# Kernel optimization log

Measured on AMD Instinct MI355X. Metric: run time of the kernel, lower is better.

## Reference

```python
import jax, jax.numpy as jnp
import numpy as np

# 3x3 window hardcoded in the original forward (symmetric, so corr == conv)
_WINDOW = np.array([[0.09474166, 0.11831801, 0.09474166],
                    [0.11831801, 0.14776132, 0.11831801],
                    [0.09474166, 0.11831801, 0.09474166]], dtype=np.float32)


def _filt(img, kern):
    # img: [B,1,H,W], kern: [1,1,3,3]; SAME padding (cv2 border effects are
    # confined to a 1-px rim, which the [5:-5,5:-5] crop removes anyway)
    return jax.lax.conv_general_dilated(
        img, kern, window_strides=(1, 1), padding='SAME',
        dimension_numbers=('NCHW', 'OIHW', 'NCHW'))


def setup_inputs() -> dict:
    key = jax.random.key(0)
    k1, k2 = jax.random.split(key)
    B, C, H, W = 64, 1, 512, 512
    X = jax.random.uniform(k1, (B, C, H, W), dtype=jnp.float32)
    Y = jax.random.uniform(k2, (B, C, H, W), dtype=jnp.float32)
    return {"X": X, "Y": Y}


def reference(X, Y):
    kern = jnp.asarray(_WINDOW)[None, None]  # [1,1,3,3]
    crop = lambda t: t[:, 0, 5:-5, 5:-5]      # channel 0, crop 5-px border

    mu1 = crop(_filt(X, kern))
    mu2 = crop(_filt(Y, kern))
    sigma1_sq = crop(_filt(X * X, kern)) - mu1 * mu1
    sigma2_sq = crop(_filt(Y * Y, kern)) - mu2 * mu2
    sigma12 = crop(_filt(X * Y, kern)) - mu1 * mu2

    # per-sample loss = mean over cropped HW; batch_loss = sum over samples
    loss = sigma1_sq * sigma2_sq - 2.0 * sigma12  # [B, H-10, W-10]
    return jnp.sum(jnp.mean(loss, axis=(1, 2)))
```

## Files before the change

### kernel.cpp

```cpp
#include <hip/hip_runtime.h>

#define A_W 0.30780133f
#define B_W 0.38439735f

#define IMG_W 512
#define CROP_LO 5
#define CROP_HI 507
#define STRIP 32
#define NSTRIPS 16
#define NCOLBLK 2
#define BLOCK_THREADS 256

struct Raw6 { float xl, xc, xr, yl, yc, yr; };
struct H5   { float s1, s2, s11, s22, s12; };

__device__ __forceinline__ Raw6 ld_row(const float* __restrict__ Xb,
                                       const float* __restrict__ Yb,
                                       int row, int c) {
    const float* Xr = Xb + (size_t)row * IMG_W;
    const float* Yr = Yb + (size_t)row * IMG_W;
    Raw6 r;
    r.xl = Xr[c - 1]; r.xc = Xr[c]; r.xr = Xr[c + 1];
    r.yl = Yr[c - 1]; r.yc = Yr[c]; r.yr = Yr[c + 1];
    return r;
}

__device__ __forceinline__ H5 hsum(const Raw6& r) {
    H5 h;
    h.s1  = A_W * (r.xl + r.xr)               + B_W * r.xc;
    h.s2  = A_W * (r.yl + r.yr)               + B_W * r.yc;
    h.s11 = A_W * (r.xl * r.xl + r.xr * r.xr) + B_W * (r.xc * r.xc);
    h.s22 = A_W * (r.yl * r.yl + r.yr * r.yr) + B_W * (r.yc * r.yc);
    h.s12 = A_W * (r.xl * r.yl + r.xr * r.yr) + B_W * (r.xc * r.yc);
    return h;
}

__global__ __launch_bounds__(BLOCK_THREADS) void ssim_loss_main(
    const float* __restrict__ X, const float* __restrict__ Y,
    float* __restrict__ partials) {
    const int t  = threadIdx.x;
    const int c  = CROP_LO + blockIdx.x * BLOCK_THREADS + t;
    const int cc = min(c, IMG_W - 2);
    const float vm = (c < CROP_HI) ? 1.0f : 0.0f;
    const int b  = blockIdx.z;
    const int i0 = CROP_LO + blockIdx.y * STRIP;

    const float* Xb = X + (size_t)b * IMG_W * IMG_W;
    const float* Yb = Y + (size_t)b * IMG_W * IMG_W;

    Raw6 rA = ld_row(Xb, Yb, i0 - 1, cc);
    Raw6 rB = ld_row(Xb, Yb, i0,     cc);
    Raw6 rC = ld_row(Xb, Yb, i0 + 1, cc);
    Raw6 rD = ld_row(Xb, Yb, i0 + 2, cc);
    H5 P = hsum(rA);
    H5 C = hsum(rB);

    float acc = 0.0f;
#pragma unroll
    for (int r = 0; r < STRIP; ++r) {
        Raw6 rNew = ld_row(Xb, Yb, min(i0 + r + 3, IMG_W - 1), cc);

        H5 N = hsum(rC);

        float s1  = A_W * (P.s1  + N.s1)  + B_W * C.s1;
        float s2  = A_W * (P.s2  + N.s2)  + B_W * C.s2;
        float s11 = A_W * (P.s11 + N.s11) + B_W * C.s11;
        float s22 = A_W * (P.s22 + N.s22) + B_W * C.s22;
        float s12 = A_W * (P.s12 + N.s12) + B_W * C.s12;

        float v1 = s11 - s1 * s1;
        float v2 = s22 - s2 * s2;
        float cv = s12 - s1 * s2;
        float term = v1 * v2 - 2.0f * cv;

        acc += (i0 + r < CROP_HI) ? vm * term : 0.0f;

        P = C; C = N; rC = rD; rD = rNew;
    }

    for (int off = 32; off > 0; off >>= 1) acc += __shfl_down(acc, off, 64);
    __shared__ float wsum[BLOCK_THREADS / 64];
    if ((t & 63) == 0) wsum[t >> 6] = acc;
    __syncthreads();
    if (t == 0)
        partials[blockIdx.x + NCOLBLK * (blockIdx.y + NSTRIPS * blockIdx.z)] =
            wsum[0] + wsum[1] + wsum[2] + wsum[3];
}

__global__ __launch_bounds__(256) void ssim_loss_finalize(
    const float* __restrict__ partials, int n, float* __restrict__ out) {
    const int tid = threadIdx.x;
    float s = 0.0f;
    for (int i = tid; i < n; i += 256) s += partials[i];
    for (int off = 32; off > 0; off >>= 1) s += __shfl_down(s, off, 64);
    __shared__ float wsum[4];
    if ((tid & 63) == 0) wsum[tid >> 6] = s;
    __syncthreads();
    if (tid == 0) {
        float total = wsum[0] + wsum[1] + wsum[2] + wsum[3];
        out[0] = total * (1.0f / 252004.0f);
    }
}

extern "C" void kernel_launch(void* const* d_in, const int* in_sizes, int n_in,
                              void* d_out, int out_size, void* d_ws, size_t ws_size,
                              hipStream_t stream) {
    const float* X = (const float*)d_in[0];
    const float* Y = (const float*)d_in[1];
    float* out = (float*)d_out;
    float* partials = (float*)d_ws;

    dim3 grid(NCOLBLK, NSTRIPS, 64);
    ssim_loss_main<<<grid, BLOCK_THREADS, 0, stream>>>(X, Y, partials);
    ssim_loss_finalize<<<1, 256, 0, stream>>>(partials, NCOLBLK * NSTRIPS * 64, out);
}
```

Measured before the change: 29.87 us.

## Stage X/Y tiles in LDS with float4 loads, two columns per thread

Each block now cooperatively loads a 34-row by 136-column halo tile of X and Y into shared memory using float4 global loads. Threads then compute two adjacent columns over 8 rows each, reading from LDS. Previously each thread issued scalar global loads for three neighbouring columns per row. The change aims to cut redundant global traffic and improve load vectorisation. In exchange it adds a block barrier, about 37KB of LDS per block that may limit occupancy, and halo rows re-read across strips.

```diff
diff --git a/kernel.cpp b/kernel.cpp
--- a/kernel.cpp
+++ b/kernel.cpp
@@ -3,88 +3,117 @@
 #define A_W 0.30780133f
 #define B_W 0.38439735f
 
-#define IMG_W 512
 #define CROP_LO 5
 #define CROP_HI 507
-#define STRIP 32
-#define NSTRIPS 16
-#define NCOLBLK 2
-#define BLOCK_THREADS 256
+#define BT 256
 
-struct Raw6 { float xl, xc, xr, yl, yc, yr; };
-struct H5   { float s1, s2, s11, s22, s12; };
+#define LROWF4 34
+#define LROWF  136
+#define IMGF4  1156
+#define IMGF   4624
 
-__device__ __forceinline__ Raw6 ld_row(const float* __restrict__ Xb,
-                                       const float* __restrict__ Yb,
-                                       int row, int c) {
-    const float* Xr = Xb + (size_t)row * IMG_W;
-    const float* Yr = Yb + (size_t)row * IMG_W;
-    Raw6 r;
-    r.xl = Xr[c - 1]; r.xc = Xr[c]; r.xr = Xr[c + 1];
-    r.yl = Yr[c - 1]; r.yc = Yr[c]; r.yr = Yr[c + 1];
-    return r;
+struct H10 { float s1[2], s2[2], s11[2], s22[2], s12[2]; };
+
+__device__ __forceinline__ void hsum2(const float x[4], const float y[4], H10& h) {
+#pragma unroll
+    for (int k = 0; k < 2; ++k) {
+        float xl = x[k], xc = x[k + 1], xr = x[k + 2];
+        float yl = y[k], yc = y[k + 1], yr = y[k + 2];
+        h.s1[k]  = A_W * (xl + xr)           + B_W * xc;
+        h.s2[k]  = A_W * (yl + yr)           + B_W * yc;
+        h.s11[k] = A_W * (xl * xl + xr * xr) + B_W * (xc * xc);
+        h.s22[k] = A_W * (yl * yl + yr * yr) + B_W * (yc * yc);
+        h.s12[k] = A_W * (xl * yl + xr * yr) + B_W * (xc * yc);
+    }
 }
 
-__device__ __forceinline__ H5 hsum(const Raw6& r) {
-    H5 h;
-    h.s1  = A_W * (r.xl + r.xr)               + B_W * r.xc;
-    h.s2  = A_W * (r.yl + r.yr)               + B_W * r.yc;
-    h.s11 = A_W * (r.xl * r.xl + r.xr * r.xr) + B_W * (r.xc * r.xc);
-    h.s22 = A_W * (r.yl * r.yl + r.yr * r.yr) + B_W * (r.yc * r.yc);
-    h.s12 = A_W * (r.xl * r.yl + r.xr * r.yr) + B_W * (r.xc * r.yc);
-    return h;
-}
-
-__global__ __launch_bounds__(BLOCK_THREADS) void ssim_loss_main(
+__global__ __launch_bounds__(BT, 4) void ssim_loss_main(
     const float* __restrict__ X, const float* __restrict__ Y,
     float* __restrict__ partials) {
+    __shared__ float4 tile4[2 * IMGF4];
+
     const int t  = threadIdx.x;
-    const int c  = CROP_LO + blockIdx.x * BLOCK_THREADS + t;
-    const int cc = min(c, IMG_W - 2);
-    const float vm = (c < CROP_HI) ? 1.0f : 0.0f;
+    const int bx = blockIdx.x;
+    const int sy = blockIdx.y;
     const int b  = blockIdx.z;
-    const int i0 = CROP_LO + blockIdx.y * STRIP;
+    const int c0 = 128 * bx;
+    const int i0 = CROP_LO + 32 * sy;
 
-    const float* Xb = X + (size_t)b * IMG_W * IMG_W;
-    const float* Yb = Y + (size_t)b * IMG_W * IMG_W;
+    const float4* X4 = (const float4*)X;
+    const float4* Y4 = (const float4*)Y;
+    const int ib = b * 65536;
 
-    Raw6 rA = ld_row(Xb, Yb, i0 - 1, cc);
-    Raw6 rB = ld_row(Xb, Yb, i0,     cc);
-    Raw6 rC = ld_row(Xb, Yb, i0 + 1, cc);
-    Raw6 rD = ld_row(Xb, Yb, i0 + 2, cc);
-    H5 P = hsum(rA);
-    H5 C = hsum(rB);
+#pragma unroll
+    for (int img = 0; img < 2; ++img) {
+        const float4* src = img ? Y4 : X4;
+#pragma unroll
+        for (int k = 0; k < 5; ++k) {
+            int f = t + BT * k;
+            if (f < IMGF4) {
+                int row = f / LROWF4;
+                int c4  = f - row * LROWF4;
+                int gr  = min(i0 - 1 + row, 511);
+                int g4  = min(max(32 * bx - 1 + c4, 0), 127);
+                tile4[img * IMGF4 + f] = src[ib + gr * 128 + g4];
+            }
+        }
+    }
+    __syncthreads();
+
+    const float* L = (const float*)tile4;
+    const int cg  = t & 63;
+    const int rs  = t >> 6;
+    const int lr0 = 8 * rs;
+    const int or0 = i0 + 8 * rs;
+    const int lcol = 2 * cg + 3;
+
+    float cm0, cm1;
+    {
+        int gc0 = c0 + 2 * cg, gc1 = gc0 + 1;
+        cm0 = (gc0 >= CROP_LO && gc0 < CROP_HI) ? 1.0f : 0.0f;
+        cm1 = (gc1 >= CROP_LO && gc1 < CROP_HI) ? 1.0f : 0.0f;
+    }
+
+    auto ldrow = [&](int img, int lr, float v[4]) {
+        const float* P = L + img * IMGF + lr * LROWF + lcol;
+        v[0] = P[0];
+        float2 m = *(const float2*)(P + 1);
+        v[1] = m.x; v[2] = m.y;
+        v[3] = P[3];
+    };
+
+    H10 Ph, Ch, Nh;
+    float x[4], y[4];
+    ldrow(0, lr0, x);     ldrow(1, lr0, y);     hsum2(x, y, Ph);
+    ldrow(0, lr0 + 1, x); ldrow(1, lr0 + 1, y); hsum2(x, y, Ch);
 
     float acc = 0.0f;
 #pragma unroll
-    for (int r = 0; r < STRIP; ++r) {
-        Raw6 rNew = ld_row(Xb, Yb, min(i0 + r + 3, IMG_W - 1), cc);
-
-        H5 N = hsum(rC);
-
-        float s1  = A_W * (P.s1  + N.s1)  + B_W * C.s1;
-        float s2  = A_W * (P.s2  + N.s2)  + B_W * C.s2;
-        float s11 = A_W * (P.s11 + N.s11) + B_W * C.s11;
-        float s22 = A_W * (P.s22 + N.s22) + B_W * C.s22;
-        float s12 = A_W * (P.s12 + N.s12) + B_W * C.s12;
-
-        float v1 = s11 - s1 * s1;
-        float v2 = s22 - s2 * s2;
-        float cv = s12 - s1 * s2;
-        float term = v1 * v2 - 2.0f * cv;
-
-        acc += (i0 + r < CROP_HI) ? vm * term : 0.0f;
-
-        P = C; C = N; rC = rD; rD = rNew;
+    for (int rr = 0; rr < 8; ++rr) {
+        ldrow(0, lr0 + 2 + rr, x); ldrow(1, lr0 + 2 + rr, y); hsum2(x, y, Nh);
+        float racc = 0.0f;
+#pragma unroll
+        for (int k = 0; k < 2; ++k) {
+            float s1  = A_W * (Ph.s1[k]  + Nh.s1[k])  + B_W * Ch.s1[k];
+            float s2  = A_W * (Ph.s2[k]  + Nh.s2[k])  + B_W * Ch.s2[k];
+            float s11 = A_W * (Ph.s11[k] + Nh.s11[k]) + B_W * Ch.s11[k];
+            float s22 = A_W * (Ph.s22[k] + Nh.s22[k]) + B_W * Ch.s22[k];
+            float s12 = A_W * (Ph.s12[k] + Nh.s12[k]) + B_W * Ch.s12[k];
+            float v1 = s11 - s1 * s1;
+            float v2 = s22 - s2 * s2;
+            float cv = s12 - s1 * s2;
+            racc += (k ? cm1 : cm0) * (v1 * v2 - 2.0f * cv);
+        }
+        acc += (or0 + rr < CROP_HI) ? racc : 0.0f;
+        Ph = Ch; Ch = Nh;
     }
 
     for (int off = 32; off > 0; off >>= 1) acc += __shfl_down(acc, off, 64);
-    __shared__ float wsum[BLOCK_THREADS / 64];
+    __shared__ float wsum[BT / 64];
     if ((t & 63) == 0) wsum[t >> 6] = acc;
     __syncthreads();
     if (t == 0)
-        partials[blockIdx.x + NCOLBLK * (blockIdx.y + NSTRIPS * blockIdx.z)] =
-            wsum[0] + wsum[1] + wsum[2] + wsum[3];
+        partials[bx + 4 * (sy + 16 * b)] = wsum[0] + wsum[1] + wsum[2] + wsum[3];
 }
 
 __global__ __launch_bounds__(256) void ssim_loss_finalize(
@@ -110,7 +139,7 @@
     float* out = (float*)d_out;
     float* partials = (float*)d_ws;
 
-    dim3 grid(NCOLBLK, NSTRIPS, 64);
-    ssim_loss_main<<<grid, BLOCK_THREADS, 0, stream>>>(X, Y, partials);
-    ssim_loss_finalize<<<1, 256, 0, stream>>>(partials, NCOLBLK * NSTRIPS * 64, out);
+    dim3 grid(4, 16, 64);
+    ssim_loss_main<<<grid, BT, 0, stream>>>(X, Y, partials);
+    ssim_loss_finalize<<<1, 256, 0, stream>>>(partials, 4096, out);
 }
```

Result: slower. 47.64 us (+59.5%).

## Compute two columns per thread with float2 loads and wave shuffles for halos

Applied to the files above, without the earlier changes.

Each thread now handles two adjacent columns across the whole 512-wide row, loading float2 from X and Y. The left and right neighbours come from wavefront shuffles instead of redundant global loads, with edge lanes falling back to scalar loads. This drops the three-loads-per-value redundancy and the wasted column block. Strips are shortened to 16 rows with twice as many of them, giving the same block count but more halo-row overhead per strip.

```diff
diff --git a/kernel.cpp b/kernel.cpp
--- a/kernel.cpp
+++ b/kernel.cpp
@@ -6,85 +6,85 @@
 #define IMG_W 512
 #define CROP_LO 5
 #define CROP_HI 507
-#define STRIP 32
-#define NSTRIPS 16
-#define NCOLBLK 2
-#define BLOCK_THREADS 256
+#define STRIP 16
+#define NSTRIPS 32
+#define BT 256
 
-struct Raw6 { float xl, xc, xr, yl, yc, yr; };
-struct H5   { float s1, s2, s11, s22, s12; };
+struct H10 { float a1[2], a2[2], a11[2], a22[2], a12[2]; };
 
-__device__ __forceinline__ Raw6 ld_row(const float* __restrict__ Xb,
-                                       const float* __restrict__ Yb,
-                                       int row, int c) {
-    const float* Xr = Xb + (size_t)row * IMG_W;
-    const float* Yr = Yb + (size_t)row * IMG_W;
-    Raw6 r;
-    r.xl = Xr[c - 1]; r.xc = Xr[c]; r.xr = Xr[c + 1];
-    r.yl = Yr[c - 1]; r.yc = Yr[c]; r.yr = Yr[c + 1];
-    return r;
-}
-
-__device__ __forceinline__ H5 hsum(const Raw6& r) {
-    H5 h;
-    h.s1  = A_W * (r.xl + r.xr)               + B_W * r.xc;
-    h.s2  = A_W * (r.yl + r.yr)               + B_W * r.yc;
-    h.s11 = A_W * (r.xl * r.xl + r.xr * r.xr) + B_W * (r.xc * r.xc);
-    h.s22 = A_W * (r.yl * r.yl + r.yr * r.yr) + B_W * (r.yc * r.yc);
-    h.s12 = A_W * (r.xl * r.yl + r.xr * r.yr) + B_W * (r.xc * r.yc);
-    return h;
-}
-
-__global__ __launch_bounds__(BLOCK_THREADS) void ssim_loss_main(
+__global__ __launch_bounds__(BT) void ssim_loss_main(
     const float* __restrict__ X, const float* __restrict__ Y,
     float* __restrict__ partials) {
     const int t  = threadIdx.x;
-    const int c  = CROP_LO + blockIdx.x * BLOCK_THREADS + t;
-    const int cc = min(c, IMG_W - 2);
-    const float vm = (c < CROP_HI) ? 1.0f : 0.0f;
-    const int b  = blockIdx.z;
-    const int i0 = CROP_LO + blockIdx.y * STRIP;
+    const int l  = t & 63;
+    const int w  = t >> 6;
+    const int c0 = 128 * w + 2 * l;
+    const int b  = blockIdx.y;
+    const int i0 = CROP_LO + STRIP * blockIdx.x;
 
     const float* Xb = X + (size_t)b * IMG_W * IMG_W;
     const float* Yb = Y + (size_t)b * IMG_W * IMG_W;
 
-    Raw6 rA = ld_row(Xb, Yb, i0 - 1, cc);
-    Raw6 rB = ld_row(Xb, Yb, i0,     cc);
-    Raw6 rC = ld_row(Xb, Yb, i0 + 1, cc);
-    Raw6 rD = ld_row(Xb, Yb, i0 + 2, cc);
-    H5 P = hsum(rA);
-    H5 C = hsum(rB);
+    const float cm0 = (c0     >= CROP_LO && c0     < CROP_HI) ? 1.0f : 0.0f;
+    const float cm1 = (c0 + 1 >= CROP_LO && c0 + 1 < CROP_HI) ? 1.0f : 0.0f;
+    const int clh = max(c0 - 1, 0);
+    const int crh = min(c0 + 2, IMG_W - 1);
+
+    auto hrow = [&](int row, H10& h) {
+        const float* Xr = Xb + (size_t)row * IMG_W;
+        const float* Yr = Yb + (size_t)row * IMG_W;
+        float2 x = *(const float2*)(Xr + c0);
+        float2 y = *(const float2*)(Yr + c0);
+        float xl = __shfl_up(x.y, 1, 64);
+        float yl = __shfl_up(y.y, 1, 64);
+        float xr = __shfl_down(x.x, 1, 64);
+        float yr = __shfl_down(y.x, 1, 64);
+        if (l == 0)  { xl = Xr[clh]; yl = Yr[clh]; }
+        if (l == 63) { xr = Xr[crh]; yr = Yr[crh]; }
+        h.a1[0]  = A_W * (xl + x.y)             + B_W * x.x;
+        h.a1[1]  = A_W * (x.x + xr)             + B_W * x.y;
+        h.a2[0]  = A_W * (yl + y.y)             + B_W * y.x;
+        h.a2[1]  = A_W * (y.x + yr)             + B_W * y.y;
+        h.a11[0] = A_W * (xl * xl + x.y * x.y)  + B_W * (x.x * x.x);
+        h.a11[1] = A_W * (x.x * x.x + xr * xr)  + B_W * (x.y * x.y);
+        h.a22[0] = A_W * (yl * yl + y.y * y.y)  + B_W * (y.x * y.x);
+        h.a22[1] = A_W * (y.x * y.x + yr * yr)  + B_W * (y.y * y.y);
+        h.a12[0] = A_W * (xl * yl + x.y * y.y)  + B_W * (x.x * y.x);
+        h.a12[1] = A_W * (x.x * y.x + xr * yr)  + B_W * (x.y * y.y);
+    };
+
+    H10 P, C, N;
+    hrow(i0 - 1, P);
+    hrow(i0,     C);
 
     float acc = 0.0f;
 #pragma unroll
-    for (int r = 0; r < STRIP; ++r) {
-        Raw6 rNew = ld_row(Xb, Yb, min(i0 + r + 3, IMG_W - 1), cc);
+    for (int rr = 0; rr < STRIP; ++rr) {
+        hrow(min(i0 + rr + 1, IMG_W - 1), N);
 
-        H5 N = hsum(rC);
-
-        float s1  = A_W * (P.s1  + N.s1)  + B_W * C.s1;
-        float s2  = A_W * (P.s2  + N.s2)  + B_W * C.s2;
-        float s11 = A_W * (P.s11 + N.s11) + B_W * C.s11;
-        float s22 = A_W * (P.s22 + N.s22) + B_W * C.s22;
-        float s12 = A_W * (P.s12 + N.s12) + B_W * C.s12;
-
-        float v1 = s11 - s1 * s1;
-        float v2 = s22 - s2 * s2;
-        float cv = s12 - s1 * s2;
-        float term = v1 * v2 - 2.0f * cv;
-
-        acc += (i0 + r < CROP_HI) ? vm * term : 0.0f;
-
-        P = C; C = N; rC = rD; rD = rNew;
+        float racc = 0.0f;
+#pragma unroll
+        for (int k = 0; k < 2; ++k) {
+            float s1  = A_W * (P.a1[k]  + N.a1[k])  + B_W * C.a1[k];
+            float s2  = A_W * (P.a2[k]  + N.a2[k])  + B_W * C.a2[k];
+            float s11 = A_W * (P.a11[k] + N.a11[k]) + B_W * C.a11[k];
+            float s22 = A_W * (P.a22[k] + N.a22[k]) + B_W * C.a22[k];
+            float s12 = A_W * (P.a12[k] + N.a12[k]) + B_W * C.a12[k];
+            float v1 = s11 - s1 * s1;
+            float v2 = s22 - s2 * s2;
+            float cv = s12 - s1 * s2;
+            racc += (k ? cm1 : cm0) * (v1 * v2 - 2.0f * cv);
+        }
+        acc += (i0 + rr < CROP_HI) ? racc : 0.0f;
+        P = C; C = N;
     }
 
     for (int off = 32; off > 0; off >>= 1) acc += __shfl_down(acc, off, 64);
-    __shared__ float wsum[BLOCK_THREADS / 64];
-    if ((t & 63) == 0) wsum[t >> 6] = acc;
+    __shared__ float wsum[BT / 64];
+    if (l == 0) wsum[w] = acc;
     __syncthreads();
     if (t == 0)
-        partials[blockIdx.x + NCOLBLK * (blockIdx.y + NSTRIPS * blockIdx.z)] =
-            wsum[0] + wsum[1] + wsum[2] + wsum[3];
+        partials[blockIdx.x + NSTRIPS * b] = wsum[0] + wsum[1] + wsum[2] + wsum[3];
 }
 
 __global__ __launch_bounds__(256) void ssim_loss_finalize(
@@ -110,7 +110,7 @@
     float* out = (float*)d_out;
     float* partials = (float*)d_ws;
 
-    dim3 grid(NCOLBLK, NSTRIPS, 64);
-    ssim_loss_main<<<grid, BLOCK_THREADS, 0, stream>>>(X, Y, partials);
-    ssim_loss_finalize<<<1, 256, 0, stream>>>(partials, NCOLBLK * NSTRIPS * 64, out);
+    dim3 grid(NSTRIPS, 64);
+    ssim_loss_main<<<grid, BT, 0, stream>>>(X, Y, partials);
+    ssim_loss_finalize<<<1, 256, 0, stream>>>(partials, NSTRIPS * 64, out);
 }
```

Measured after the change: 43.51 us. 1.46x slower.
